# Performance work log

Measured on AMD Instinct MI355X. Metric: run time of the kernel, lower is better.

## Reference

```python
import jax, jax.numpy as jnp
import numpy as np

B, T, D, H = 32, 1024, 512, 512


def setup_inputs() -> dict:
    key = jax.random.key(0)
    k = jax.random.split(key, 5)
    s = 1.0 / np.sqrt(H)  # PyTorch LSTM init scale U(-1/sqrt(H), 1/sqrt(H))
    return {
        "x": jax.random.normal(k[0], (B, T, D), dtype=jnp.float32),
        "W_ih": jax.random.uniform(k[1], (4 * H, D), jnp.float32, -s, s),
        "W_hh": jax.random.uniform(k[2], (4 * H, H), jnp.float32, -s, s),
        "b_ih": jax.random.uniform(k[3], (4 * H,), jnp.float32, -s, s),
        "b_hh": jax.random.uniform(k[4], (4 * H,), jnp.float32, -s, s),
    }


def _lstm(x, W_ih, W_hh, b_ih, b_hh):
    # x: [B, T, D] (batch_first). Precompute input projections for all steps.
    xg = jnp.einsum("btd,gd->btg", x, W_ih) + (b_ih + b_hh)  # [B, T, 4H]
    xg = jnp.transpose(xg, (1, 0, 2))  # [T, B, 4H] time-major for scan

    def step(carry, xg_t):
        h, c = carry  # [B, H] each
        gates = xg_t + h @ W_hh.T  # [B, 4H]
        i, f, g, o = jnp.split(gates, 4, axis=-1)  # PyTorch gate order i,f,g,o
        i = jax.nn.sigmoid(i)
        f = jax.nn.sigmoid(f)
        g = jnp.tanh(g)
        o = jax.nn.sigmoid(o)
        c = f * c + i * g
        h = o * jnp.tanh(c)
        return (h, c), h

    h0 = jnp.zeros((x.shape[0], H), x.dtype)
    c0 = jnp.zeros((x.shape[0], H), x.dtype)
    (h_n, c_n), hs = jax.lax.scan(step, (h0, c0), xg)
    out = jnp.transpose(hs, (1, 0, 2))  # [B, T, H] batch_first output
    return out, h_n[None], c_n[None]  # h_n/c_n: [num_layers=1, B, H]


def reference(x, W_ih, W_hh, b_ih, b_hh):
    # Returns (last_hidden_state, h_n, c_n) matching outputs[0], outputs[1]
    return _lstm(x, W_ih, W_hh, b_ih, b_hh)
```

## Files before the change

### kernel.cpp

```cpp
#include <hip/hip_runtime.h>
#include <stdint.h>

typedef __attribute__((ext_vector_type(4))) float f32x4;
typedef __attribute__((ext_vector_type(8))) short bf16x8;
typedef __attribute__((ext_vector_type(4))) unsigned int u32x4;
typedef __attribute__((ext_vector_type(2))) unsigned int u32x2;
typedef __attribute__((ext_vector_type(4))) unsigned short u16x4;
typedef unsigned short ushort_t;

#define B_N 32
#define T_N 1024
#define D_N 512
#define H_N 512
#define G4H 2048

__device__ __forceinline__ ushort_t f2bf(float f) {
    union { float f; unsigned int u; } v; v.f = f;
    unsigned int r = v.u + 0x7FFFu + ((v.u >> 16) & 1u);
    return (ushort_t)(r >> 16);
}
__device__ __forceinline__ float bf2f(ushort_t b) {
    union { unsigned int u; float f; } v; v.u = ((unsigned int)b) << 16;
    return v.f;
}
__device__ __forceinline__ float fsig(float x) {
    return __builtin_amdgcn_rcpf(1.f + __expf(-x));
}
__device__ __forceinline__ float ftanh(float x) {
    return 1.f - 2.f * __builtin_amdgcn_rcpf(1.f + __expf(2.f * x));
}

__global__ __launch_bounds__(256) void prep_kernel(
    const float* __restrict__ x, const float* __restrict__ wih,
    const float* __restrict__ whh, const float* __restrict__ bih,
    const float* __restrict__ bhh,
    ushort_t* __restrict__ xb, ushort_t* __restrict__ wihb,
    ushort_t* __restrict__ whhb, float* __restrict__ bias,
    unsigned int* __restrict__ ringu)
{
    size_t i = (size_t)blockIdx.x * 256 + threadIdx.x;
    if (i < 2048) bias[i] = bih[i] + bhh[i];
    if (i < 32768) ringu[i] = 0u;
    const size_t NX = (size_t)B_N * T_N * D_N / 4;
    const size_t NW = (size_t)G4H * D_N / 4;
    if (i < NX) {
        f32x4 v = ((const f32x4*)x)[i];
        u16x4 o; o[0]=f2bf(v[0]); o[1]=f2bf(v[1]); o[2]=f2bf(v[2]); o[3]=f2bf(v[3]);
        ((u16x4*)xb)[i] = o;
    } else if (i < NX + NW) {
        size_t j = i - NX;
        f32x4 v = ((const f32x4*)wih)[j];
        u16x4 o; o[0]=f2bf(v[0]); o[1]=f2bf(v[1]); o[2]=f2bf(v[2]); o[3]=f2bf(v[3]);
        ((u16x4*)wihb)[j] = o;
    } else if (i < NX + 2 * NW) {
        size_t j = i - NX - NW;
        f32x4 v = ((const f32x4*)whh)[j];
        u16x4 o; o[0]=f2bf(v[0]); o[1]=f2bf(v[1]); o[2]=f2bf(v[2]); o[3]=f2bf(v[3]);
        ((u16x4*)whhb)[j] = o;
    }
}

__global__ __launch_bounds__(512) void xg_gemm(
    const ushort_t* __restrict__ xb,
    const ushort_t* __restrict__ wihb,
    const float* __restrict__ bias,
    ushort_t* __restrict__ xg)
{
    int blk = blockIdx.x;
    int tc = blk >> 4;
    int gb = blk & 15;
    int w  = threadIdx.x >> 6;
    int l  = threadIdx.x & 63;
    int lr = l & 15;
    int lk = l >> 4;

    int arow = gb * 128 + w * 16 + lr;
    const ushort_t* ap = wihb + (size_t)arow * D_N;

    f32x4 acc[16];
#pragma unroll
    for (int i = 0; i < 16; ++i) { acc[i][0]=0.f; acc[i][1]=0.f; acc[i][2]=0.f; acc[i][3]=0.f; }

#pragma unroll
    for (int kk = 0; kk < 16; ++kk) {
        bf16x8 af = *(const bf16x8*)(ap + kk * 32 + lk * 8);
#pragma unroll
        for (int nn = 0; nn < 16; ++nn) {
            int tl = nn >> 1, bh = nn & 1;
            int bcol = bh * 16 + lr;
            int t = tc * 8 + tl;
            bf16x8 bf = *(const bf16x8*)(xb + ((size_t)bcol * T_N + t) * D_N + kk * 32 + lk * 8);
            acc[nn] = __builtin_amdgcn_mfma_f32_16x16x32_bf16(af, bf, acc[nn], 0, 0, 0);
        }
    }

    float bs[4];
#pragma unroll
    for (int j = 0; j < 4; ++j) bs[j] = bias[gb * 128 + w * 16 + lk * 4 + j];

#pragma unroll
    for (int nn = 0; nn < 16; ++nn) {
        int tl = nn >> 1, bh = nn & 1;
        int bcol = bh * 16 + lr;
        int t = tc * 8 + tl;
#pragma unroll
        for (int j = 0; j < 4; ++j) {
            int r = gb * 128 + w * 16 + lk * 4 + j;
            xg[((size_t)t * G4H + r) * B_N + bcol] = f2bf(acc[nn][j] + bs[j]);
        }
    }
}

__global__ __launch_bounds__(512, 1) void lstm_rec(
    const ushort_t* __restrict__ xg,
    const ushort_t* __restrict__ whhb,
    unsigned int* __restrict__ ringu,
    float* __restrict__ out,
    float* __restrict__ hn,
    float* __restrict__ cn)
{
    const int tid = threadIdx.x;
    const int g = blockIdx.x >> 4;
    const int s = blockIdx.x & 15;
    const int w = tid >> 6, l = tid & 63, lr = l & 15, lk = l >> 4;

    __shared__ ushort_t hstage[4][544];

    const int col4 = s * 32 + w * 4;
    const int gc = (lr >> 2) * 512 + col4 + (lr & 3);
    bf16x8 wfrag[16];
#pragma unroll
    for (int kk = 0; kk < 16; ++kk)
        wfrag[kk] = *(const bf16x8*)(whhb + (size_t)gc * H_N + kk * 32 + lk * 8);

    float c_reg[4] = {0.f, 0.f, 0.f, 0.f};
    unsigned int* ringg = ringu + g * 4096;
    const ushort_t* xgp = xg + (size_t)gc * B_N + g * 4;

    for (int t = 0; t < T_N; ++t) {
        u32x2 xv = *(const u32x2*)(xgp + (size_t)t * (G4H * B_N));
        f32x4 acc0, acc1;
        union { u32x2 u; ushort_t s4[4]; } xu; xu.u = xv;
#pragma unroll
        for (int j = 0; j < 4; ++j) { acc0[j] = bf2f(xu.s4[j]); acc1[j] = 0.f; }

        if (t > 0) {
            if (tid < 64) {
                const unsigned int* pp0 = ringg + ((t - 1) & 1) * 2048 + l * 8;
                const unsigned int* pp1 = pp0 + 1024;
                const unsigned int tp = ((unsigned int)t) << 16;
                u32x4 a[8];
                int guard = 0;
                for (;;) {
                    asm volatile(
                        "global_load_dwordx4 %0, %8, off sc0 sc1\n\t"
                        "global_load_dwordx4 %1, %8, off offset:16 sc0 sc1\n\t"
                        "global_load_dwordx4 %2, %8, off offset:2048 sc0 sc1\n\t"
                        "global_load_dwordx4 %3, %8, off offset:2064 sc0 sc1\n\t"
                        "global_load_dwordx4 %4, %9, off sc0 sc1\n\t"
                        "global_load_dwordx4 %5, %9, off offset:16 sc0 sc1\n\t"
                        "global_load_dwordx4 %6, %9, off offset:2048 sc0 sc1\n\t"
                        "global_load_dwordx4 %7, %9, off offset:2064 sc0 sc1\n\t"
                        "s_waitcnt vmcnt(0)"
                        : "=&v"(a[0]), "=&v"(a[1]), "=&v"(a[2]), "=&v"(a[3]),
                          "=&v"(a[4]), "=&v"(a[5]), "=&v"(a[6]), "=&v"(a[7])
                        : "v"(pp0), "v"(pp1)
                        : "memory");
                    unsigned int d = 0;
#pragma unroll
                    for (int r = 0; r < 8; ++r) {
                        d |= (a[r][0] ^ tp); d |= (a[r][1] ^ tp);
                        d |= (a[r][2] ^ tp); d |= (a[r][3] ^ tp);
                    }
                    int ok = ((d & 0xFFFF0000u) == 0u);
                    if (__all(ok) || ++guard > (1 << 16)) break;
                    __builtin_amdgcn_s_sleep(1);
                }
#pragma unroll
                for (int n = 0; n < 4; ++n) {
                    u32x4 p;
                    p[0] = __builtin_amdgcn_perm(a[2*n][1], a[2*n][0], 0x05040100u);
                    p[1] = __builtin_amdgcn_perm(a[2*n][3], a[2*n][2], 0x05040100u);
                    p[2] = __builtin_amdgcn_perm(a[2*n+1][1], a[2*n+1][0], 0x05040100u);
                    p[3] = __builtin_amdgcn_perm(a[2*n+1][3], a[2*n+1][2], 0x05040100u);
                    *(u32x4*)((char*)hstage + n * 1088 + l * 16) = p;
                }
            }
            __syncthreads();

            const char* ap = (const char*)hstage + (lr & 3) * 1088 + lk * 16;
#pragma unroll
            for (int kk = 0; kk < 16; ++kk) {
                bf16x8 af = *(const bf16x8*)(ap + kk * 64);
                if (kk & 1)
                    acc1 = __builtin_amdgcn_mfma_f32_16x16x32_bf16(af, wfrag[kk], acc1, 0, 0, 0);
                else
                    acc0 = __builtin_amdgcn_mfma_f32_16x16x32_bf16(af, wfrag[kk], acc0, 0, 0, 0);
            }
        } else {
            __syncthreads();
        }

#pragma unroll
        for (int j = 0; j < 4; ++j) acc0[j] += acc1[j];

        const int q = (l >> 2) & 3;
        float av[4];
#pragma unroll
        for (int j = 0; j < 4; ++j)
            av[j] = (q == 2) ? ftanh(acc0[j]) : fsig(acc0[j]);

        float hv[4];
#pragma unroll
        for (int j = 0; j < 4; ++j) {
            float f_ = __shfl_xor(av[j], 4);
            float g_ = __shfl_xor(av[j], 8);
            float o_ = __shfl_xor(av[j], 12);
            c_reg[j] = f_ * c_reg[j] + av[j] * g_;
            hv[j] = o_ * ftanh(c_reg[j]);
        }

        if (l < 4) {
            unsigned int* rp = ringg + (t & 1) * 2048 + col4 + l;
            const unsigned int tag = ((unsigned int)(t + 1)) << 16;
#pragma unroll
            for (int j = 0; j < 4; ++j) {
                unsigned int hw = tag | (unsigned int)f2bf(hv[j]);
                asm volatile("global_store_dword %0, %1, off sc0 sc1"
                             :: "v"(rp + j * 512), "v"(hw) : "memory");
            }
            float* op = out + (size_t)(g * 4) * T_N * H_N + (size_t)t * H_N + col4 + l;
#pragma unroll
            for (int j = 0; j < 4; ++j)
                op[(size_t)j * T_N * H_N] = hv[j];
            if (t == T_N - 1) {
#pragma unroll
                for (int j = 0; j < 4; ++j) {
                    size_t bi = (size_t)(g * 4 + j) * H_N + col4 + l;
                    hn[bi] = hv[j];
                    cn[bi] = c_reg[j];
                }
            }
        }
    }
}

extern "C" void kernel_launch(void* const* d_in, const int* in_sizes, int n_in,
                              void* d_out, int out_size, void* d_ws, size_t ws_size,
                              hipStream_t stream) {
    (void)in_sizes; (void)n_in; (void)out_size; (void)ws_size;
    const float* x   = (const float*)d_in[0];
    const float* wih = (const float*)d_in[1];
    const float* whh = (const float*)d_in[2];
    const float* bih = (const float*)d_in[3];
    const float* bhh = (const float*)d_in[4];
    float* out = (float*)d_out;
    float* hn  = out + (size_t)B_N * T_N * H_N;
    float* cn  = hn + (size_t)B_N * H_N;

    char* ws = (char*)d_ws;
    ushort_t*     xg    = (ushort_t*)    (ws);
    ushort_t*     xb    = (ushort_t*)    (ws + 134217728);
    ushort_t*     wihb  = (ushort_t*)    (ws + 167772160);
    ushort_t*     whhb  = (ushort_t*)    (ws + 169869312);
    float*        bias  = (float*)       (ws + 171966464);
    unsigned int* ringu = (unsigned int*)(ws + 171974656);

    prep_kernel<<<18432, 256, 0, stream>>>(x, wih, whh, bih, bhh,
                                           xb, wihb, whhb, bias, ringu);
    xg_gemm<<<2048, 512, 0, stream>>>(xb, wihb, bias, xg);
    lstm_rec<<<128, 512, 0, stream>>>(xg, whhb, ringu, out, hn, cn);
}
```

Measured before the change: 2.673 ms.

## Fuse x bf16 conversion into input GEMM and switch xg to batch-major layout

The separate fp32-to-bf16 pass over x is removed. The input-projection GEMM now reads fp32 x directly, converts it into LDS tiles, keeps W_ih fragments in registers for two 128-row blocks, and loops over the batch. The xg layout changes from [t][gate][b] to [t][b][gate] so the GEMM writes contiguous 4-element vectors. In exchange, the recurrent kernel now does four strided scalar loads per step instead of one vector load.

```diff
diff --git a/kernel.cpp b/kernel.cpp
--- a/kernel.cpp
+++ b/kernel.cpp
@@ -31,83 +31,89 @@
 }
 
 __global__ __launch_bounds__(256) void prep_kernel(
-    const float* __restrict__ x, const float* __restrict__ wih,
-    const float* __restrict__ whh, const float* __restrict__ bih,
-    const float* __restrict__ bhh,
-    ushort_t* __restrict__ xb, ushort_t* __restrict__ wihb,
-    ushort_t* __restrict__ whhb, float* __restrict__ bias,
-    unsigned int* __restrict__ ringu)
+    const float* __restrict__ wih, const float* __restrict__ whh,
+    const float* __restrict__ bih, const float* __restrict__ bhh,
+    ushort_t* __restrict__ wihb, ushort_t* __restrict__ whhb,
+    float* __restrict__ bias, unsigned int* __restrict__ ringu)
 {
     size_t i = (size_t)blockIdx.x * 256 + threadIdx.x;
     if (i < 2048) bias[i] = bih[i] + bhh[i];
     if (i < 32768) ringu[i] = 0u;
-    const size_t NX = (size_t)B_N * T_N * D_N / 4;
     const size_t NW = (size_t)G4H * D_N / 4;
-    if (i < NX) {
-        f32x4 v = ((const f32x4*)x)[i];
+    if (i < NW) {
+        f32x4 v = ((const f32x4*)wih)[i];
         u16x4 o; o[0]=f2bf(v[0]); o[1]=f2bf(v[1]); o[2]=f2bf(v[2]); o[3]=f2bf(v[3]);
-        ((u16x4*)xb)[i] = o;
-    } else if (i < NX + NW) {
-        size_t j = i - NX;
-        f32x4 v = ((const f32x4*)wih)[j];
-        u16x4 o; o[0]=f2bf(v[0]); o[1]=f2bf(v[1]); o[2]=f2bf(v[2]); o[3]=f2bf(v[3]);
-        ((u16x4*)wihb)[j] = o;
-    } else if (i < NX + 2 * NW) {
-        size_t j = i - NX - NW;
+        ((u16x4*)wihb)[i] = o;
+    } else if (i < 2 * NW) {
+        size_t j = i - NW;
         f32x4 v = ((const f32x4*)whh)[j];
         u16x4 o; o[0]=f2bf(v[0]); o[1]=f2bf(v[1]); o[2]=f2bf(v[2]); o[3]=f2bf(v[3]);
         ((u16x4*)whhb)[j] = o;
     }
 }
 
-__global__ __launch_bounds__(512) void xg_gemm(
-    const ushort_t* __restrict__ xb,
+__global__ __launch_bounds__(512, 1) void xg_gemm(
+    const float* __restrict__ x,
     const ushort_t* __restrict__ wihb,
     const float* __restrict__ bias,
     ushort_t* __restrict__ xg)
 {
-    int blk = blockIdx.x;
-    int tc = blk >> 4;
-    int gb = blk & 15;
-    int w  = threadIdx.x >> 6;
-    int l  = threadIdx.x & 63;
-    int lr = l & 15;
-    int lk = l >> 4;
-
-    int arow = gb * 128 + w * 16 + lr;
-    const ushort_t* ap = wihb + (size_t)arow * D_N;
-
-    f32x4 acc[16];
-#pragma unroll
-    for (int i = 0; i < 16; ++i) { acc[i][0]=0.f; acc[i][1]=0.f; acc[i][2]=0.f; acc[i][3]=0.f; }
-
+    const int tc = blockIdx.x >> 3;
+    const int gb = blockIdx.x & 7;
+    const int tid = threadIdx.x;
+    const int w = tid >> 6, l = tid & 63, lr = l & 15, lk = l >> 4;
+
+    __shared__ ushort_t xs[16 * 520];
+
+    const int r0 = gb * 256 + w * 16;
+    const int r1 = r0 + 128;
+    bf16x8 a0[16], a1[16];
 #pragma unroll
     for (int kk = 0; kk < 16; ++kk) {
-        bf16x8 af = *(const bf16x8*)(ap + kk * 32 + lk * 8);
-#pragma unroll
-        for (int nn = 0; nn < 16; ++nn) {
-            int tl = nn >> 1, bh = nn & 1;
-            int bcol = bh * 16 + lr;
-            int t = tc * 8 + tl;
-            bf16x8 bf = *(const bf16x8*)(xb + ((size_t)bcol * T_N + t) * D_N + kk * 32 + lk * 8);
-            acc[nn] = __builtin_amdgcn_mfma_f32_16x16x32_bf16(af, bf, acc[nn], 0, 0, 0);
-        }
-    }
-
-    float bs[4];
-#pragma unroll
-    for (int j = 0; j < 4; ++j) bs[j] = bias[gb * 128 + w * 16 + lk * 4 + j];
-
-#pragma unroll
-    for (int nn = 0; nn < 16; ++nn) {
-        int tl = nn >> 1, bh = nn & 1;
-        int bcol = bh * 16 + lr;
-        int t = tc * 8 + tl;
+        a0[kk] = *(const bf16x8*)(wihb + (size_t)(r0 + lr) * D_N + kk * 32 + lk * 8);
+        a1[kk] = *(const bf16x8*)(wihb + (size_t)(r1 + lr) * D_N + kk * 32 + lk * 8);
+    }
+    float bs0[4], bs1[4];
+#pragma unroll
+    for (int j = 0; j < 4; ++j) {
+        bs0[j] = bias[r0 + lk * 4 + j];
+        bs1[j] = bias[r1 + lk * 4 + j];
+    }
+
+    const int srow = tid >> 5;
+    const int sq   = tid & 31;
+
+    for (int b = 0; b < B_N; ++b) {
+        const float* xr = x + ((size_t)b * T_N + tc * 16 + srow) * D_N;
+#pragma unroll
+        for (int c = 0; c < 4; ++c) {
+            f32x4 v = *(const f32x4*)(xr + c * 128 + sq * 4);
+            u16x4 o; o[0]=f2bf(v[0]); o[1]=f2bf(v[1]); o[2]=f2bf(v[2]); o[3]=f2bf(v[3]);
+            *(u16x4*)(xs + srow * 520 + c * 128 + sq * 4) = o;
+        }
+        __syncthreads();
+
+        f32x4 c0, c1;
+#pragma unroll
+        for (int j = 0; j < 4; ++j) { c0[j] = 0.f; c1[j] = 0.f; }
+#pragma unroll
+        for (int kk = 0; kk < 16; ++kk) {
+            bf16x8 bf = *(const bf16x8*)((const char*)xs + lr * 1040 + kk * 64 + lk * 16);
+            c0 = __builtin_amdgcn_mfma_f32_16x16x32_bf16(a0[kk], bf, c0, 0, 0, 0);
+            c1 = __builtin_amdgcn_mfma_f32_16x16x32_bf16(a1[kk], bf, c1, 0, 0, 0);
+        }
+
+        const int t = tc * 16 + lr;
+        ushort_t* op = xg + (size_t)t * (B_N * G4H) + (size_t)b * G4H;
+        u16x4 o0, o1;
 #pragma unroll
         for (int j = 0; j < 4; ++j) {
-            int r = gb * 128 + w * 16 + lk * 4 + j;
-            xg[((size_t)t * G4H + r) * B_N + bcol] = f2bf(acc[nn][j] + bs[j]);
-        }
+            o0[j] = f2bf(c0[j] + bs0[j]);
+            o1[j] = f2bf(c1[j] + bs1[j]);
+        }
+        *(u16x4*)(op + r0 + lk * 4) = o0;
+        *(u16x4*)(op + r1 + lk * 4) = o1;
+        __syncthreads();
     }
 }
 
@@ -135,14 +141,16 @@
 
     float c_reg[4] = {0.f, 0.f, 0.f, 0.f};
     unsigned int* ringg = ringu + g * 4096;
-    const ushort_t* xgp = xg + (size_t)gc * B_N + g * 4;
+    const ushort_t* xgp = xg + (size_t)(g * 4) * G4H + gc;
 
     for (int t = 0; t < T_N; ++t) {
-        u32x2 xv = *(const u32x2*)(xgp + (size_t)t * (G4H * B_N));
+        const ushort_t* xa = xgp + (size_t)t * (B_N * G4H);
         f32x4 acc0, acc1;
-        union { u32x2 u; ushort_t s4[4]; } xu; xu.u = xv;
-#pragma unroll
-        for (int j = 0; j < 4; ++j) { acc0[j] = bf2f(xu.s4[j]); acc1[j] = 0.f; }
+#pragma unroll
+        for (int j = 0; j < 4; ++j) {
+            acc0[j] = bf2f(xa[(size_t)j * G4H]);
+            acc1[j] = 0.f;
+        }
 
         if (t > 0) {
             if (tid < 64) {
@@ -260,14 +268,13 @@
 
     char* ws = (char*)d_ws;
     ushort_t*     xg    = (ushort_t*)    (ws);
-    ushort_t*     xb    = (ushort_t*)    (ws + 134217728);
     ushort_t*     wihb  = (ushort_t*)    (ws + 167772160);
     ushort_t*     whhb  = (ushort_t*)    (ws + 169869312);
     float*        bias  = (float*)       (ws + 171966464);
     unsigned int* ringu = (unsigned int*)(ws + 171974656);
 
-    prep_kernel<<<18432, 256, 0, stream>>>(x, wih, whh, bih, bhh,
-                                           xb, wihb, whhb, bias, ringu);
-    xg_gemm<<<2048, 512, 0, stream>>>(xb, wihb, bias, xg);
+    prep_kernel<<<2048, 256, 0, stream>>>(wih, whh, bih, bhh,
+                                          wihb, whhb, bias, ringu);
+    xg_gemm<<<512, 512, 0, stream>>>(x, wihb, bias, xg);
     lstm_rec<<<128, 512, 0, stream>>>(xg, whhb, ringu, out, hn, cn);
 }
```

Result: faster. 2.276 ms (-14.9%).
